# Optimization experiments

Measured on AMD Instinct MI355X. Metric: run time of the kernel, lower is better.

## Reference

```python
import jax, jax.numpy as jnp
import numpy as np

CODEBOOK_SIZE = 8192
TOKEN_SIZE = 256
BETA = 0.25


def setup_inputs() -> dict:
    key = jax.random.key(0)
    kx, kc = jax.random.split(key)
    x = jax.random.normal(kx, (32, TOKEN_SIZE, 32, 32), dtype=jnp.float32)
    # torch init: uniform_(-1/K, 1/K)
    codebook = jax.random.uniform(
        kc, (CODEBOOK_SIZE, TOKEN_SIZE), dtype=jnp.float32,
        minval=-1.0 / CODEBOOK_SIZE, maxval=1.0 / CODEBOOK_SIZE)
    return {"x": x, "codebook": codebook}


def reference(x, codebook):
    sg = jax.lax.stop_gradient
    B, C, H, W = x.shape  # C == TOKEN_SIZE
    xt = jnp.transpose(x, (0, 2, 3, 1))           # [B,H,W,C]
    xf = xt.reshape(-1, C)                         # [N,C]
    d = (jnp.sum(xf * xf, axis=1, keepdims=True)
         + jnp.sum(codebook * codebook, axis=1)
         - 2.0 * jnp.einsum('nd,kd->nk', xf, codebook))
    min_encoding_indices = jnp.argmin(d, axis=1)   # [N]
    min_encodings = jax.nn.one_hot(min_encoding_indices, codebook.shape[0],
                                   dtype=x.dtype)  # [N,K]
    x_quantized = codebook[min_encoding_indices].reshape(xt.shape)  # [B,H,W,C]
    loss = (BETA * jnp.mean(sg(xt) - x_quantized)
            + jnp.mean((xt - sg(x_quantized)) ** 2))
    # straight-through estimator
    x_quantized = xt + sg(x_quantized - xt)
    e_mean = jnp.mean(min_encodings, axis=0)
    perplexity = jnp.exp(-jnp.sum(e_mean * jnp.log(e_mean + 1e-10)))
    x_quantized = jnp.transpose(x_quantized, (0, 3, 1, 2))  # [B,C,H,W]
    return (x_quantized, loss, perplexity, min_encodings,
            min_encoding_indices[:, None])
```

## Files before the change

kernel.cpp:

```cpp
#include <hip/hip_runtime.h>
#include <hip/hip_bf16.h>


#define TOK   32768
#define KCB   8192
#define CDIM  256

#define LOSS_OFF   8388608
#define PERP_OFF   8388609
#define OH_OFF     8388610
#define OH_ELEMS   268435456
#define IDX_OFF    276824066

#define NTILES_K   64

typedef _Float16 f16x8 __attribute__((ext_vector_type(8)));
typedef _Float16 f16x4 __attribute__((ext_vector_type(4)));
typedef float    f32x4 __attribute__((ext_vector_type(4)));

#define BSCALE     8192.0f
#define BSCALE_INV 0x1p-13f

__device__ __forceinline__ void gload16(const void* g, void* l) {
    __builtin_amdgcn_global_load_lds(
        (const __attribute__((address_space(1))) void*)g,
        (__attribute__((address_space(3))) void*)l, 16, 0, 0);
}

__global__ __launch_bounds__(256) void s_kernel(const float* __restrict__ x,
                                                float* __restrict__ S) {
    int n = blockIdx.x * 256 + threadIdx.x;
    int b = n >> 10, hw = n & 1023;
    const float* p = x + (size_t)b * 262144 + hw;
    double s = 0.0;
    #pragma unroll 8
    for (int c = 0; c < CDIM; ++c) {
        float v = p[(size_t)c * 1024];
        s += (double)v * (double)v;
    }
    S[n] = (float)s;
}

__global__ __launch_bounds__(256) void split_x_kernel(const float* __restrict__ x,
                                                      _Float16* __restrict__ A16) {
    __shared__ float xs[64][65];
    const int n0 = blockIdx.x * 64;
    const int b = n0 >> 10, hw0 = n0 & 1023;
    const float* xb = x + (size_t)b * 262144 + hw0;
    const int cr = threadIdx.x >> 6, i = threadIdx.x & 63;
    const int tl = threadIdx.x >> 2, part = threadIdx.x & 3;

    for (int ch = 0; ch < 4; ++ch) {
        const int c0 = ch * 64;
        __syncthreads();
        #pragma unroll
        for (int j = 0; j < 16; ++j)
            xs[cr * 16 + j][i] = xb[(size_t)(c0 + cr * 16 + j) * 1024 + i];
        __syncthreads();
        f16x8 h0, h1, l0, l1;
        #pragma unroll
        for (int j = 0; j < 8; ++j) {
            float v = xs[part * 16 + j][tl];
            _Float16 h = (_Float16)v;
            h0[j] = h; l0[j] = (_Float16)(v - (float)h);
        }
        #pragma unroll
        for (int j = 0; j < 8; ++j) {
            float v = xs[part * 16 + 8 + j][tl];
            _Float16 h = (_Float16)v;
            h1[j] = h; l1[j] = (_Float16)(v - (float)h);
        }
        _Float16* dst = A16 + (size_t)(n0 + tl) * 512 + c0 + part * 16;
        *(f16x8*)(dst)           = h0;
        *(f16x8*)(dst + 8)       = h1;
        *(f16x8*)(dst + 256)     = l0;
        *(f16x8*)(dst + 256 + 8) = l1;
    }
}

__global__ __launch_bounds__(256) void split_cb_kernel(const float* __restrict__ cb,
                                                       _Float16* __restrict__ B16) {
    int t = blockIdx.x * 256 + threadIdx.x;
    int code = t >> 6, c = (t & 63) * 4;
    float4 v = *(const float4*)(cb + (size_t)code * 256 + c);
    float ev[4] = {v.x * BSCALE, v.y * BSCALE, v.z * BSCALE, v.w * BSCALE};
    f16x4 h, l;
    #pragma unroll
    for (int j = 0; j < 4; ++j) {
        _Float16 hh = (_Float16)ev[j];
        h[j] = hh; l[j] = (_Float16)(ev[j] - (float)hh);
    }
    *(f16x4*)(B16 + (size_t)code * 512 + c)       = h;
    *(f16x4*)(B16 + (size_t)code * 512 + 256 + c) = l;
}

__global__ __launch_bounds__(256) void dist_mfma_kernel(
        const _Float16* __restrict__ A16, const _Float16* __restrict__ B16,
        const float* __restrict__ S,
        float* __restrict__ pd, int* __restrict__ pi) {
    __shared__ char smem[32768];
    __shared__ float dred[128][2];
    __shared__ int   kred[128][2];

    const int tid  = threadIdx.x;
    const int lane = tid & 63, w = tid >> 6;
    const int wr = w >> 1, wc = w & 1;
    const int m0 = blockIdx.y * 128, n0 = blockIdx.x * 128;

    char* As = smem;
    char* Bs = smem + 16384;

    const int srow   = lane >> 3;
    const int schunk = (lane & 7) ^ (lane >> 3);

    f32x4 acc[4][4] = {};

    const int arow = wr * 64 + (lane & 15);
    const int brow = wc * 64 + (lane & 15);
    const int kb   = (lane >> 4) * 16;

    for (int s = 0; s < 12; ++s) {
        const int ph = s >> 2, r = (s & 3) * 64;
        const int aK = (ph == 2 ? 256 : 0) + r;
        const int bK = (ph == 1 ? 256 : 0) + r;
        __syncthreads();
        #pragma unroll
        for (int t = 0; t < 4; ++t) {
            const int row = w * 32 + t * 8 + srow;
            const int L   = w * 4096 + t * 1024 + lane * 16;
            gload16((const char*)A16 + (size_t)(m0 + row) * 1024 + aK * 2 + schunk * 16, As + L);
            gload16((const char*)B16 + (size_t)(n0 + row) * 1024 + bK * 2 + schunk * 16, Bs + L);
        }
        __syncthreads();
        #pragma unroll
        for (int kk = 0; kk < 2; ++kk) {
            f16x8 af[4], bf[4];
            #pragma unroll
            for (int m = 0; m < 4; ++m) {
                const int rr = arow + m * 16;
                int off = rr * 128 + kk * 64 + kb;
                off ^= (rr & 7) << 4;
                af[m] = *(const f16x8*)(As + off);
            }
            #pragma unroll
            for (int n = 0; n < 4; ++n) {
                const int rr = brow + n * 16;
                int off = rr * 128 + kk * 64 + kb;
                off ^= (rr & 7) << 4;
                bf[n] = *(const f16x8*)(Bs + off);
            }
            #pragma unroll
            for (int m = 0; m < 4; ++m)
                #pragma unroll
                for (int n = 0; n < 4; ++n)
                    acc[m][n] = __builtin_amdgcn_mfma_f32_16x16x32_f16(
                        af[m], bf[n], acc[m][n], 0, 0, 0);
        }
    }

    #pragma unroll
    for (int m = 0; m < 4; ++m) {
        #pragma unroll
        for (int reg = 0; reg < 4; ++reg) {
            const int rloc = wr * 64 + m * 16 + (lane >> 4) * 4 + reg;
            const float Sv = S[m0 + rloc];
            float bd = 3.4e38f; int bk = 0x7fffffff;
            #pragma unroll
            for (int n = 0; n < 4; ++n) {
                float dot = acc[m][n][reg] * BSCALE_INV;
                float d = fmaf(-2.0f, dot, Sv);
                const int col = n0 + wc * 64 + n * 16 + (lane & 15);
                if (d < bd) { bd = d; bk = col; }
            }
            #pragma unroll
            for (int msk = 1; msk < 16; msk <<= 1) {
                float od = __shfl_xor(bd, msk, 64);
                int   ok = __shfl_xor(bk, msk, 64);
                if (od < bd || (od == bd && ok < bk)) { bd = od; bk = ok; }
            }
            if ((lane & 15) == 0) { dred[rloc][wc] = bd; kred[rloc][wc] = bk; }
        }
    }
    __syncthreads();
    if (tid < 128) {
        float d0 = dred[tid][0], d1 = dred[tid][1];
        int   k0 = kred[tid][0], k1 = kred[tid][1];
        bool take1 = (d1 < d0) || (d1 == d0 && k1 < k0);
        pd[(size_t)blockIdx.x * TOK + m0 + tid] = take1 ? d1 : d0;
        pi[(size_t)blockIdx.x * TOK + m0 + tid] = take1 ? k1 : k0;
    }
}

__global__ __launch_bounds__(256) void argmin_reduce_kernel(
        const float* __restrict__ pd, const int* __restrict__ pi,
        int* __restrict__ idx, unsigned* __restrict__ counts,
        float* __restrict__ out_idxf) {
    int n = blockIdx.x * 256 + threadIdx.x;
    float bestd = 3.4e38f;
    int   bestk = 0x7fffffff;
    for (int t = 0; t < NTILES_K; ++t) {
        float d = pd[(size_t)t * TOK + n];
        int   k = pi[(size_t)t * TOK + n];
        if (d < bestd || (d == bestd && k < bestk)) { bestd = d; bestk = k; }
    }
    idx[n] = bestk;
    out_idxf[n] = (float)bestk;
    atomicAdd(&counts[bestk], 1u);
}

__global__ __launch_bounds__(256) void onehot_fill_kernel(
        const int* __restrict__ idx, float* __restrict__ oh) {
    const size_t tid0 = (size_t)blockIdx.x * 256 + threadIdx.x;
    for (int it = 0; it < 32; ++it) {
        size_t e4 = tid0 + (size_t)it * 2097152;
        size_t f0 = e4 * 4;
        int n = (int)(f0 >> 13);
        int k = (int)(f0 & 8191);
        float4 z = make_float4(0.f, 0.f, 0.f, 0.f);
        int id = idx[n];
        int dlt = id - k;
        if (dlt >= 0 && dlt < 4) ((float*)&z)[dlt] = 1.0f;
        *(float4*)(oh + f0) = z;
    }
}

__global__ __launch_bounds__(256) void xq_loss_kernel(
        const float* __restrict__ x, const float* __restrict__ cb,
        const int* __restrict__ idx, float* __restrict__ xq,
        double* __restrict__ accum) {
    __shared__ float qs[64][65];
    __shared__ double r1s[4], r2s[4];
    const int n0 = blockIdx.x * 64;
    const int b = n0 >> 10, hw0 = n0 & 1023;
    const float* xb  = x  + (size_t)b * 262144 + hw0;
    float*       xqb = xq + (size_t)b * 262144 + hw0;
    const int cr = threadIdx.x >> 6, i = threadIdx.x & 63;
    const int tl = threadIdx.x >> 2, part = threadIdx.x & 3;
    const int myidx = idx[n0 + tl];
    double s1 = 0.0, s2 = 0.0;

    for (int ch = 0; ch < 4; ++ch) {
        const int c0 = ch * 64;
        __syncthreads();
        #pragma unroll
        for (int j = 0; j < 4; ++j) {
            float4 q = *(const float4*)(cb + (size_t)myidx * 256 + c0 + part * 16 + j * 4);
            qs[part * 16 + j * 4 + 0][tl] = q.x;
            qs[part * 16 + j * 4 + 1][tl] = q.y;
            qs[part * 16 + j * 4 + 2][tl] = q.z;
            qs[part * 16 + j * 4 + 3][tl] = q.w;
        }
        __syncthreads();
        #pragma unroll
        for (int j = 0; j < 16; ++j) {
            const int c = c0 + cr * 16 + j;
            float xv = xb[(size_t)c * 1024 + i];
            float qv = qs[cr * 16 + j][i];
            float t = qv - xv;
            xqb[(size_t)c * 1024 + i] = xv + t;
            float d = xv - qv;
            s1 += (double)d;
            s2 += (double)d * (double)d;
        }
    }

    #pragma unroll
    for (int m = 1; m < 64; m <<= 1) {
        s1 += __shfl_xor(s1, m, 64);
        s2 += __shfl_xor(s2, m, 64);
    }
    const int wv = threadIdx.x >> 6, ln = threadIdx.x & 63;
    if (ln == 0) { r1s[wv] = s1; r2s[wv] = s2; }
    __syncthreads();
    if (threadIdx.x == 0) {
        atomicAdd(&accum[0], r1s[0] + r1s[1] + r1s[2] + r1s[3]);
        atomicAdd(&accum[1], r2s[0] + r2s[1] + r2s[2] + r2s[3]);
    }
}

__global__ __launch_bounds__(256) void finalize_kernel(
        const unsigned* __restrict__ counts, const double* __restrict__ accum,
        float* __restrict__ out) {
    double h = 0.0;
    for (int k = threadIdx.x; k < KCB; k += 256) {
        float e = (float)counts[k] / 32768.0f;
        h += (double)(e * logf(e + 1e-10f));
    }
    #pragma unroll
    for (int m = 1; m < 64; m <<= 1) h += __shfl_xor(h, m, 64);
    __shared__ double rh[4];
    int wv = threadIdx.x >> 6, ln = threadIdx.x & 63;
    if (ln == 0) rh[wv] = h;
    __syncthreads();
    if (threadIdx.x == 0) {
        double H = rh[0] + rh[1] + rh[2] + rh[3];
        double m1 = accum[0] / 8388608.0;
        double m2 = accum[1] / 8388608.0;
        out[LOSS_OFF] = (float)(0.25 * m1 + m2);
        out[PERP_OFF] = expf((float)(-H));
    }
}

extern "C" void kernel_launch(void* const* d_in, const int* in_sizes, int n_in,
                              void* d_out, int out_size, void* d_ws, size_t ws_size,
                              hipStream_t stream) {
    const float* x  = (const float*)d_in[0];
    const float* cb = (const float*)d_in[1];
    float* out = (float*)d_out;
    char*  ws  = (char*)d_ws;

    float*    S      = (float*)ws;
    int*      idx    = (int*)(ws + 131072);
    unsigned* counts = (unsigned*)(ws + 262144);
    double*   accum  = (double*)(ws + 294912);

    float* out_xq   = out;
    float* out_oh   = out + OH_OFF;
    float* out_idxf = out + IDX_OFF;

    char* stg = (char*)d_out + ((((size_t)OH_OFF * 4) + 255) & ~(size_t)255);
    float*    pd  = (float*)stg;
    int*      pi  = (int*)(stg + (8u << 20));
    _Float16* A16 = (_Float16*)(stg + (16u << 20));
    _Float16* B16 = (_Float16*)(stg + (48u << 20));

    hipMemsetAsync(ws + 262144, 0, 32768 + 16, stream);

    s_kernel<<<128, 256, 0, stream>>>(x, S);
    split_x_kernel<<<512, 256, 0, stream>>>(x, A16);
    split_cb_kernel<<<2048, 256, 0, stream>>>(cb, B16);
    dist_mfma_kernel<<<dim3(64, 256), 256, 0, stream>>>(A16, B16, S, pd, pi);
    argmin_reduce_kernel<<<128, 256, 0, stream>>>(pd, pi, idx, counts, out_idxf);
    onehot_fill_kernel<<<8192, 256, 0, stream>>>(idx, out_oh);
    xq_loss_kernel<<<512, 256, 0, stream>>>(x, cb, idx, out_xq, accum);
    finalize_kernel<<<1, 256, 0, stream>>>(counts, accum, out);
}
```

Before: 1.994 ms.

## Pipeline distance GEMM with 3-stage LDS ring, larger tiles and swizzled grid

Rewrites the distance MFMA kernel to use 128x256 tiles with 8 waves. Global-to-LDS loads are triple-buffered and prefetched two stages ahead, with explicit waitcnt, barriers and priority hints so loads overlap with MFMA work. The block order is swizzled for cache reuse, and partial argmin outputs are halved. The one-hot fill also switches to nontemporal stores to avoid polluting the cache. The large LDS footprint limits occupancy to one block per CU, and the manual waitcnt counting is fragile.

After: 1.996 ms. Within noise of the previous version (+0.1%).

```diff
diff --git a/kernel.cpp b/kernel.cpp
--- a/kernel.cpp
+++ b/kernel.cpp
@@ -12,7 +12,7 @@
 #define OH_ELEMS   268435456
 #define IDX_OFF    276824066
 
-#define NTILES_K   64
+#define NTILES_K   32
 
 typedef _Float16 f16x8 __attribute__((ext_vector_type(8)));
 typedef _Float16 f16x4 __attribute__((ext_vector_type(4)));
@@ -94,82 +94,151 @@
     *(f16x4*)(B16 + (size_t)code * 512 + 256 + c) = l;
 }
 
-__global__ __launch_bounds__(256) void dist_mfma_kernel(
+__global__ __launch_bounds__(512, 2) void dist_mfma_kernel(
         const _Float16* __restrict__ A16, const _Float16* __restrict__ B16,
         const float* __restrict__ S,
         float* __restrict__ pd, int* __restrict__ pi) {
-    __shared__ char smem[32768];
-    __shared__ float dred[128][2];
-    __shared__ int   kred[128][2];
+    __shared__ char smem[147456];
 
     const int tid  = threadIdx.x;
     const int lane = tid & 63, w = tid >> 6;
-    const int wr = w >> 1, wc = w & 1;
-    const int m0 = blockIdx.y * 128, n0 = blockIdx.x * 128;
-
-    char* As = smem;
-    char* Bs = smem + 16384;
-
-    const int srow   = lane >> 3;
-    const int schunk = (lane & 7) ^ (lane >> 3);
+    const int wr = w >> 2, wc = w & 3;
+
+    const int id  = (int)(blockIdx.y * gridDim.x + blockIdx.x);
+    const int nid = (id & 7) * 1024 + (id >> 3);
+    const int bxt = nid >> 8;
+    const int byt = nid & 255;
+    const int m0  = byt * 128;
+    const int n0  = bxt * 256;
+
+    const char* A16b = (const char*)A16;
+    const char* B16b = (const char*)B16;
+
+    const int srow     = tid >> 3;
+    const int schunk16 = ((tid & 7) ^ (srow & 7)) << 4;
+
+    const int lr  = lane & 15;
+    const int l47 = lane & 7;
+    const int lhi = lane >> 4;
 
     f32x4 acc[4][4] = {};
 
-    const int arow = wr * 64 + (lane & 15);
-    const int brow = wc * 64 + (lane & 15);
-    const int kb   = (lane >> 4) * 16;
-
-    for (int s = 0; s < 12; ++s) {
-        const int ph = s >> 2, r = (s & 3) * 64;
-        const int aK = (ph == 2 ? 256 : 0) + r;
-        const int bK = (ph == 1 ? 256 : 0) + r;
-        __syncthreads();
-        #pragma unroll
-        for (int t = 0; t < 4; ++t) {
-            const int row = w * 32 + t * 8 + srow;
-            const int L   = w * 4096 + t * 1024 + lane * 16;
-            gload16((const char*)A16 + (size_t)(m0 + row) * 1024 + aK * 2 + schunk * 16, As + L);
-            gload16((const char*)B16 + (size_t)(n0 + row) * 1024 + bK * 2 + schunk * 16, Bs + L);
-        }
-        __syncthreads();
-        #pragma unroll
-        for (int kk = 0; kk < 2; ++kk) {
-            f16x8 af[4], bf[4];
-            #pragma unroll
-            for (int m = 0; m < 4; ++m) {
-                const int rr = arow + m * 16;
-                int off = rr * 128 + kk * 64 + kb;
-                off ^= (rr & 7) << 4;
-                af[m] = *(const f16x8*)(As + off);
+    #pragma unroll
+    for (int s = 0; s < 2; ++s) {
+        const int aK2 = s * 128, bK2 = s * 128;
+        char* Ab = smem + s * 49152;
+        char* Bb = Ab + 16384;
+        gload16(A16b + (size_t)(m0 + srow)      * 1024 + aK2 + schunk16, Ab + tid * 16);
+        gload16(A16b + (size_t)(m0 + 64 + srow) * 1024 + aK2 + schunk16, Ab + 8192 + tid * 16);
+        #pragma unroll
+        for (int i = 0; i < 4; ++i)
+            gload16(B16b + (size_t)(n0 + i * 64 + srow) * 1024 + bK2 + schunk16,
+                    Bb + i * 8192 + tid * 16);
+    }
+    asm volatile("s_waitcnt vmcnt(6)" ::: "memory");
+    __builtin_amdgcn_sched_barrier(0);
+    __builtin_amdgcn_s_barrier();
+    __builtin_amdgcn_sched_barrier(0);
+
+    #pragma unroll
+    for (int g = 0; g < 12; ++g) {
+        char* Ab = smem + (g % 3) * 49152;
+        char* Bb = Ab + 16384;
+        const int s2 = g + 2;
+        char* Ab2 = smem + (s2 % 3) * 49152;
+        char* Bb2 = Ab2 + 16384;
+        const int ph2 = s2 >> 2, rk2 = (s2 & 3) * 128;
+        const int aK2 = (ph2 == 2 ? 512 : 0) + rk2;
+        const int bK2 = (ph2 == 1 ? 512 : 0) + rk2;
+
+        f16x8 bf[4][2], af[2][2];
+        #pragma unroll
+        for (int n = 0; n < 4; ++n)
+            #pragma unroll
+            for (int kk = 0; kk < 2; ++kk) {
+                const int row = wc * 64 + n * 16 + lr;
+                bf[n][kk] = *(const f16x8*)(Bb + row * 128 + (((kk * 4 + lhi) ^ l47) << 4));
             }
-            #pragma unroll
-            for (int n = 0; n < 4; ++n) {
-                const int rr = brow + n * 16;
-                int off = rr * 128 + kk * 64 + kb;
-                off ^= (rr & 7) << 4;
-                bf[n] = *(const f16x8*)(Bs + off);
+        #pragma unroll
+        for (int m = 0; m < 2; ++m)
+            #pragma unroll
+            for (int kk = 0; kk < 2; ++kk) {
+                const int row = wr * 64 + m * 16 + lr;
+                af[m][kk] = *(const f16x8*)(Ab + row * 128 + (((kk * 4 + lhi) ^ l47) << 4));
             }
-            #pragma unroll
-            for (int m = 0; m < 4; ++m)
+        if (s2 < 12) {
+            gload16(A16b + (size_t)(m0 + srow)      * 1024 + aK2 + schunk16, Ab2 + tid * 16);
+            gload16(A16b + (size_t)(m0 + 64 + srow) * 1024 + aK2 + schunk16, Ab2 + 8192 + tid * 16);
+            gload16(B16b + (size_t)(n0 + srow)      * 1024 + bK2 + schunk16, Bb2 + tid * 16);
+        }
+        __builtin_amdgcn_s_barrier();
+        asm volatile("s_waitcnt lgkmcnt(0)" ::: "memory");
+        __builtin_amdgcn_sched_barrier(0);
+        __builtin_amdgcn_s_setprio(1);
+        #pragma unroll
+        for (int m = 0; m < 2; ++m)
+            #pragma unroll
+            for (int n = 0; n < 4; ++n)
                 #pragma unroll
-                for (int n = 0; n < 4; ++n)
+                for (int kk = 0; kk < 2; ++kk)
                     acc[m][n] = __builtin_amdgcn_mfma_f32_16x16x32_f16(
-                        af[m], bf[n], acc[m][n], 0, 0, 0);
-        }
-    }
+                        af[m][kk], bf[n][kk], acc[m][n], 0, 0, 0);
+        __builtin_amdgcn_s_setprio(0);
+        __builtin_amdgcn_sched_barrier(0);
+        __builtin_amdgcn_s_barrier();
+        __builtin_amdgcn_sched_barrier(0);
+
+        f16x8 af2[2][2];
+        #pragma unroll
+        for (int m = 0; m < 2; ++m)
+            #pragma unroll
+            for (int kk = 0; kk < 2; ++kk) {
+                const int row = wr * 64 + (m + 2) * 16 + lr;
+                af2[m][kk] = *(const f16x8*)(Ab + row * 128 + (((kk * 4 + lhi) ^ l47) << 4));
+            }
+        if (s2 < 12) {
+            #pragma unroll
+            for (int i = 1; i < 4; ++i)
+                gload16(B16b + (size_t)(n0 + i * 64 + srow) * 1024 + bK2 + schunk16,
+                        Bb2 + i * 8192 + tid * 16);
+        }
+        __builtin_amdgcn_s_barrier();
+        asm volatile("s_waitcnt lgkmcnt(0)" ::: "memory");
+        __builtin_amdgcn_sched_barrier(0);
+        __builtin_amdgcn_s_setprio(1);
+        #pragma unroll
+        for (int m = 0; m < 2; ++m)
+            #pragma unroll
+            for (int n = 0; n < 4; ++n)
+                #pragma unroll
+                for (int kk = 0; kk < 2; ++kk)
+                    acc[m + 2][n] = __builtin_amdgcn_mfma_f32_16x16x32_f16(
+                        af2[m][kk], bf[n][kk], acc[m + 2][n], 0, 0, 0);
+        __builtin_amdgcn_s_setprio(0);
+        __builtin_amdgcn_sched_barrier(0);
+
+        if (g < 10) asm volatile("s_waitcnt vmcnt(6)" ::: "memory");
+        else        asm volatile("s_waitcnt vmcnt(0)" ::: "memory");
+        __builtin_amdgcn_sched_barrier(0);
+        __builtin_amdgcn_s_barrier();
+        __builtin_amdgcn_sched_barrier(0);
+    }
+
+    float* dredf = (float*)smem;
+    int*   kredi = (int*)(smem + 2048);
 
     #pragma unroll
     for (int m = 0; m < 4; ++m) {
         #pragma unroll
         for (int reg = 0; reg < 4; ++reg) {
-            const int rloc = wr * 64 + m * 16 + (lane >> 4) * 4 + reg;
+            const int rloc = wr * 64 + m * 16 + lhi * 4 + reg;
             const float Sv = S[m0 + rloc];
             float bd = 3.4e38f; int bk = 0x7fffffff;
             #pragma unroll
             for (int n = 0; n < 4; ++n) {
                 float dot = acc[m][n][reg] * BSCALE_INV;
                 float d = fmaf(-2.0f, dot, Sv);
-                const int col = n0 + wc * 64 + n * 16 + (lane & 15);
+                const int col = n0 + wc * 64 + n * 16 + lr;
                 if (d < bd) { bd = d; bk = col; }
             }
             #pragma unroll
@@ -178,16 +247,19 @@
                 int   ok = __shfl_xor(bk, msk, 64);
                 if (od < bd || (od == bd && ok < bk)) { bd = od; bk = ok; }
             }
-            if ((lane & 15) == 0) { dred[rloc][wc] = bd; kred[rloc][wc] = bk; }
+            if (lr == 0) { dredf[rloc * 4 + wc] = bd; kredi[rloc * 4 + wc] = bk; }
         }
     }
     __syncthreads();
     if (tid < 128) {
-        float d0 = dred[tid][0], d1 = dred[tid][1];
-        int   k0 = kred[tid][0], k1 = kred[tid][1];
-        bool take1 = (d1 < d0) || (d1 == d0 && k1 < k0);
-        pd[(size_t)blockIdx.x * TOK + m0 + tid] = take1 ? d1 : d0;
-        pi[(size_t)blockIdx.x * TOK + m0 + tid] = take1 ? k1 : k0;
+        float bd = dredf[tid * 4]; int bk = kredi[tid * 4];
+        #pragma unroll
+        for (int j = 1; j < 4; ++j) {
+            float d = dredf[tid * 4 + j]; int k2 = kredi[tid * 4 + j];
+            if (d < bd || (d == bd && k2 < bk)) { bd = d; bk = k2; }
+        }
+        pd[(size_t)bxt * TOK + m0 + tid] = bd;
+        pi[(size_t)bxt * TOK + m0 + tid] = bk;
     }
 }
 
@@ -216,11 +288,11 @@
         size_t f0 = e4 * 4;
         int n = (int)(f0 >> 13);
         int k = (int)(f0 & 8191);
-        float4 z = make_float4(0.f, 0.f, 0.f, 0.f);
+        f32x4 z = {0.f, 0.f, 0.f, 0.f};
         int id = idx[n];
         int dlt = id - k;
-        if (dlt >= 0 && dlt < 4) ((float*)&z)[dlt] = 1.0f;
-        *(float4*)(oh + f0) = z;
+        if (dlt >= 0 && dlt < 4) z[dlt] = 1.0f;
+        __builtin_nontemporal_store(z, (f32x4*)(oh + f0));
     }
 }
 
@@ -320,16 +392,16 @@
 
     char* stg = (char*)d_out + ((((size_t)OH_OFF * 4) + 255) & ~(size_t)255);
     float*    pd  = (float*)stg;
-    int*      pi  = (int*)(stg + (8u << 20));
-    _Float16* A16 = (_Float16*)(stg + (16u << 20));
-    _Float16* B16 = (_Float16*)(stg + (48u << 20));
+    int*      pi  = (int*)(stg + (4u << 20));
+    _Float16* A16 = (_Float16*)(stg + (8u << 20));
+    _Float16* B16 = (_Float16*)(stg + (40u << 20));
 
     hipMemsetAsync(ws + 262144, 0, 32768 + 16, stream);
 
     s_kernel<<<128, 256, 0, stream>>>(x, S);
     split_x_kernel<<<512, 256, 0, stream>>>(x, A16);
     split_cb_kernel<<<2048, 256, 0, stream>>>(cb, B16);
-    dist_mfma_kernel<<<dim3(64, 256), 256, 0, stream>>>(A16, B16, S, pd, pi);
+    dist_mfma_kernel<<<dim3(32, 256), 512, 0, stream>>>(A16, B16, S, pd, pi);
     argmin_reduce_kernel<<<128, 256, 0, stream>>>(pd, pi, idx, counts, out_idxf);
     onehot_fill_kernel<<<8192, 256, 0, stream>>>(idx, out_oh);
     xq_loss_kernel<<<512, 256, 0, stream>>>(x, cb, idx, out_xq, accum);
```
